# Kernel tuning notes

Measured on AMD Instinct MI355X. Metric: run time of the kernel, lower is better.

## Reference

```python
import jax, jax.numpy as jnp
import numpy as np

NUM_HEADS = 8
ATTN_LEN = 5


def setup_inputs() -> dict:
    rng = jax.random.key(0)
    ks = jax.random.split(rng, 10)
    B, T, D = 2, 4096, 1024
    H, HD = NUM_HEADS, D // NUM_HEADS
    n = lambda k, shape, scale=1.0: jax.random.normal(k, shape, jnp.float32) * scale
    return {
        "query": n(ks[0], (B, T, D)),
        "key": n(ks[1], (B, T, D)),
        "value": n(ks[2], (B, T, D)),
        "Wq": n(ks[3], (D, D), 0.02),
        "bq": jnp.zeros((D,), jnp.float32),
        "Wk": n(ks[4], (D, D), 0.02),
        "bk": jnp.zeros((D,), jnp.float32),
        "Wv": n(ks[5], (D, D), 0.02),
        "bv": jnp.zeros((D,), jnp.float32),
        "Er": n(ks[6], (H, HD, ATTN_LEN)),
        "layer": 1,
    }


def _forward(query, key, value, Wq, bq, Wk, bk, Wv, bv, Er, layer):
    B, T, D = query.shape
    H = NUM_HEADS
    HD = D // H
    dil = 2 ** layer
    pad = dil * (ATTN_LEN // 2)
    Tp = T + 2 * pad

    # torch nn.Linear: y = x @ W^T + b ; reshape to [B, H, T, HD]
    q = (query @ Wq.T + bq).reshape(B, T, H, HD).transpose(0, 2, 1, 3)
    k = (key @ Wk.T + bk).reshape(B, T, H, HD).transpose(0, 2, 1, 3)
    v = (value @ Wv.T + bv).reshape(B, T, H, HD).transpose(0, 2, 1, 3)

    # head-group source mapping + shifts (note k head 7 reuses k head 6, per source)
    src_k = jnp.array([0, 1, 2, 3, 4, 5, 6, 6])
    src_v = jnp.array([0, 1, 2, 3, 4, 5, 6, 7])
    shifts = jnp.array([0, 0, 0, 0, -2, -1, 1, 2])

    # kv_roll equivalence: window slot j at time t for shift s reads
    # padded[(t + (s + j) * dil) mod Tp]  (torch.roll wraparound included)
    t_idx = jnp.arange(T)
    j_idx = jnp.arange(ATTN_LEN)
    idx = (t_idx[None, :, None] + (shifts[:, None, None] + j_idx[None, None, :]) * dil) % Tp  # [H,T,L]

    def windows(x, src):
        xp = jnp.pad(x, ((0, 0), (0, 0), (pad, pad), (0, 0)))[:, src]  # [B,H,Tp,HD]
        g = jnp.take_along_axis(xp, idx.reshape(1, H, T * ATTN_LEN, 1), axis=2)
        return g.reshape(B, H, T, ATTN_LEN, HD)

    kw = windows(k, src_k)  # [B,H,T,L,HD]
    vw = windows(v, src_v)

    qk = jnp.einsum('bhtd,bhtjd->bhtj', q, kw)            # [B,H,T,L]
    mask = jnp.where(qk == 0.0, -jnp.inf, 0.0)            # zero dot product => padding
    qer = jnp.einsum('bhtd,hdj->bhtj', q, Er)             # relative positional bias
    attn = jax.nn.softmax((qk + qer) / np.sqrt(HD).astype(np.float32) + mask, axis=-1)
    out = jnp.einsum('bhtj,bhtjd->bhtd', attn, vw)        # [B,H,T,HD]
    out = out.transpose(0, 2, 1, 3).reshape(B, T, D)
    return out, attn[:, :, :, None, :]                     # attn shaped [B,H,T,1,L] like torch


def reference(query, key, value, Wq, bq, Wk, bk, Wv, bv, Er, layer):
    return _forward(query, key, value, Wq, bq, Wk, bk, Wv, bv, Er, layer)
```

## Files before the change

kernel.cpp:

```cpp
#include <hip/hip_runtime.h>
#include <hip/hip_bf16.h>

constexpr int B_ = 2, T_ = 4096, D_ = 1024, H_ = 8, HD_ = 128, L_ = 5;
constexpr int M_ = B_ * T_;
constexpr int K_ = D_;
constexpr int N_ = D_;
constexpr int TB_ = 64;
constexpr int NSMAX_ = 96;

typedef __attribute__((ext_vector_type(8))) __bf16 bf16x8;
typedef __attribute__((ext_vector_type(4))) float f32x4;

__device__ __constant__ int c_srck[8]  = {0, 1, 2, 3, 4, 5, 6, 6};
__device__ __constant__ int c_shift[8] = {0, 0, 0, 0, -2, -1, 1, 2};

__device__ __forceinline__ void gload_lds16(const void* g, void* l) {
    __builtin_amdgcn_global_load_lds(
        (__attribute__((address_space(1))) void*)g,
        (__attribute__((address_space(3))) void*)l, 16, 0, 0);
}

__global__ __launch_bounds__(256) void qkv_gemm_f32(
    const float* __restrict__ query,
    const float* __restrict__ key,
    const float* __restrict__ value,
    const float* __restrict__ Wq,
    const float* __restrict__ bq,
    const float* __restrict__ Wk,
    const float* __restrict__ bk,
    const float* __restrict__ Wv,
    const float* __restrict__ bv,
    __hip_bfloat16* __restrict__ qout,
    __hip_bfloat16* __restrict__ kout,
    __hip_bfloat16* __restrict__ vout)
{
    const int z = blockIdx.z;
    const float* A    = (z == 0) ? query : (z == 1) ? key : value;
    const float* W    = (z == 0) ? Wq    : (z == 1) ? Wk  : Wv;
    const float* bias = (z == 0) ? bq    : (z == 1) ? bk  : bv;
    __hip_bfloat16* C = (z == 0) ? qout  : (z == 1) ? kout : vout;

    __shared__ __align__(16) float As[128 * 32];
    __shared__ __align__(16) float Bs[128 * 32];

    const int tid  = threadIdx.x;
    const int wave = tid >> 6;
    const int lane = tid & 63;
    const int m0 = blockIdx.x * 128;
    const int n0 = blockIdx.y * 128;
    const int wm = (wave >> 1) * 64;
    const int wn = (wave & 1) * 64;

    f32x4 acc[4][4];
#pragma unroll
    for (int i = 0; i < 4; ++i)
#pragma unroll
        for (int j = 0; j < 4; ++j)
            acc[i][j] = (f32x4){0.f, 0.f, 0.f, 0.f};

    const int srow = lane >> 3;
    const int lcg  = (lane & 7) ^ srow;
    const int gcol = lcg * 4;

    const int fr  = lane & 15;
    const int r7  = fr & 7;
    const int cgA = (lane >> 4) * 2;
    const int pcg0 = (cgA)     ^ r7;
    const int pcg1 = (cgA ^ 1) ^ r7;

    for (int k0 = 0; k0 < K_; k0 += 32) {
#pragma unroll
        for (int r = 0; r < 4; ++r) {
            const int issue = wave + r * 4;
            const int row = issue * 8 + srow;
            gload_lds16(A + (size_t)(m0 + row) * K_ + k0 + gcol,
                        (void*)(As + issue * 256));
            gload_lds16(W + (size_t)(n0 + row) * K_ + k0 + gcol,
                        (void*)(Bs + issue * 256));
        }
        __syncthreads();

        bf16x8 af[4], bf[4];
#pragma unroll
        for (int i = 0; i < 4; ++i) {
            const float* ap = As + (wm + i * 16 + fr) * 32;
            f32x4 a0 = *(const f32x4*)(const void*)(ap + pcg0 * 4);
            f32x4 a1 = *(const f32x4*)(const void*)(ap + pcg1 * 4);
            const float* bp = Bs + (wn + i * 16 + fr) * 32;
            f32x4 b0 = *(const f32x4*)(const void*)(bp + pcg0 * 4);
            f32x4 b1 = *(const f32x4*)(const void*)(bp + pcg1 * 4);
#pragma unroll
            for (int e = 0; e < 4; ++e) {
                af[i][e]     = (__bf16)a0[e];
                af[i][e + 4] = (__bf16)a1[e];
                bf[i][e]     = (__bf16)b0[e];
                bf[i][e + 4] = (__bf16)b1[e];
            }
        }
#pragma unroll
        for (int i = 0; i < 4; ++i)
#pragma unroll
            for (int j = 0; j < 4; ++j)
                acc[i][j] = __builtin_amdgcn_mfma_f32_16x16x32_bf16(
                    af[i], bf[j], acc[i][j], 0, 0, 0);
        __syncthreads();
    }

    const int col_l = lane & 15;
    const int row_l = (lane >> 4) * 4;
#pragma unroll
    for (int j = 0; j < 4; ++j) {
        const int n = n0 + wn + j * 16 + col_l;
        const float bval = bias[n];
#pragma unroll
        for (int i = 0; i < 4; ++i) {
            const int m = m0 + wm + i * 16 + row_l;
#pragma unroll
            for (int r = 0; r < 4; ++r)
                C[(size_t)(m + r) * N_ + n] = __float2bfloat16(acc[i][j][r] + bval);
        }
    }
}

__global__ __launch_bounds__(256) void attn_kernel(
    const __hip_bfloat16* __restrict__ qp,
    const __hip_bfloat16* __restrict__ kp,
    const __hip_bfloat16* __restrict__ vp,
    const float* __restrict__ Er,
    const int* __restrict__ layer_p,
    float* __restrict__ out,
    float* __restrict__ attn_out)
{
    const int dil = 1 << (*layer_p);
    int NS = TB_ + 4 * dil;
    if (NS > NSMAX_) NS = NSMAX_;

    const int tid = threadIdx.x;
    const int t0 = blockIdx.x * TB_;
    const int h  = blockIdx.y;
    const int b  = blockIdx.z;
    const int shift = c_shift[h];
    const int srck  = c_srck[h];
    const int off_lo = (shift - 2) * dil;

    __shared__ __align__(16) __hip_bfloat16 Ks[NSMAX_ * 128];
    __shared__ __align__(16) __hip_bfloat16 Vs[NSMAX_ * 128];
    __shared__ __align__(16) float ErT[5][128];

    for (int i = tid; i < 640; i += 256) {
        const int d = i / 5, j = i - d * 5;
        ErT[j][d] = Er[(size_t)h * 640 + i];
    }

    const int sr = tid >> 4;
    const int sc = tid & 15;
    for (int i0 = 0; i0 < NS; i0 += 16) {
        const int i = i0 + sr;
        if (i < NS) {
            const int r = t0 + off_lo + i;
            bf16x8 kv8 = (bf16x8){0, 0, 0, 0, 0, 0, 0, 0};
            bf16x8 vv8 = (bf16x8){0, 0, 0, 0, 0, 0, 0, 0};
            if (r >= 0 && r < T_) {
                kv8 = *(const bf16x8*)(const void*)(
                    kp + (size_t)(b * T_ + r) * D_ + srck * HD_ + sc * 8);
                vv8 = *(const bf16x8*)(const void*)(
                    vp + (size_t)(b * T_ + r) * D_ + h * HD_ + sc * 8);
            }
            const int pc = sc ^ (i & 3);
            *(bf16x8*)(void*)(Ks + i * 128 + pc * 8) = kv8;
            *(bf16x8*)(void*)(Vs + i * 128 + pc * 8) = vv8;
        }
    }
    __syncthreads();

    const int lr = tid >> 2;
    const int ld = tid & 3;
    const int t  = t0 + lr;
    const size_t qoff = (size_t)(b * T_ + t) * D_ + h * HD_ + ld * 32;

    float qf[32];
#pragma unroll
    for (int c = 0; c < 4; ++c) {
        bf16x8 qv = *(const bf16x8*)(const void*)(qp + qoff + c * 8);
#pragma unroll
        for (int e = 0; e < 8; ++e) qf[c * 8 + e] = (float)qv[e];
    }

    float lg[5];
    bool  valid[5];
    int   irow[5];
#pragma unroll
    for (int j = 0; j < 5; ++j) {
        const int i = lr + j * dil;
        irow[j] = i;
        const int orig = t + (shift + j - 2) * dil;
        valid[j] = (orig >= 0) && (orig < T_);

        float s = 0.f;
#pragma unroll
        for (int c = 0; c < 4; ++c) {
            const int pc = (ld * 4 + c) ^ (i & 3);
            bf16x8 kk = *(const bf16x8*)(const void*)(Ks + i * 128 + pc * 8);
#pragma unroll
            for (int e = 0; e < 8; ++e) s += qf[c * 8 + e] * (float)kk[e];
        }
        if (!valid[j]) s = 0.f;
#pragma unroll
        for (int c = 0; c < 8; ++c) {
            f32x4 ev = *(const f32x4*)(const void*)(&ErT[j][ld * 32 + c * 4]);
#pragma unroll
            for (int e = 0; e < 4; ++e) s += qf[c * 4 + e] * ev[e];
        }
        s += __shfl_xor(s, 1, 4);
        s += __shfl_xor(s, 2, 4);
        lg[j] = valid[j] ? s * 0.08838834764831845f : -INFINITY;
    }

    float mx = lg[0];
#pragma unroll
    for (int j = 1; j < 5; ++j) mx = fmaxf(mx, lg[j]);
    float w[5], sum = 0.f;
#pragma unroll
    for (int j = 0; j < 5; ++j) {
        w[j] = valid[j] ? __expf(lg[j] - mx) : 0.f;
        sum += w[j];
    }
    const float inv = 1.f / sum;
#pragma unroll
    for (int j = 0; j < 5; ++j) w[j] *= inv;

    float o[32];
#pragma unroll
    for (int m = 0; m < 32; ++m) o[m] = 0.f;
#pragma unroll
    for (int j = 0; j < 5; ++j) {
        const int i = irow[j];
#pragma unroll
        for (int c = 0; c < 4; ++c) {
            const int pc = (ld * 4 + c) ^ (i & 3);
            bf16x8 vv = *(const bf16x8*)(const void*)(Vs + i * 128 + pc * 8);
#pragma unroll
            for (int e = 0; e < 8; ++e) o[c * 8 + e] += w[j] * (float)vv[e];
        }
    }

#pragma unroll
    for (int c = 0; c < 8; ++c) {
        f32x4 ov = (f32x4){o[c * 4], o[c * 4 + 1], o[c * 4 + 2], o[c * 4 + 3]};
        *(f32x4*)(void*)(out + qoff + c * 4) = ov;
    }

    const size_t abase = ((size_t)(b * H_ + h) * T_ + t) * L_;
    attn_out[abase + ld] = w[ld];
    if (ld == 0) attn_out[abase + 4] = w[4];
}

extern "C" void kernel_launch(void* const* d_in, const int* in_sizes, int n_in,
                              void* d_out, int out_size, void* d_ws, size_t ws_size,
                              hipStream_t stream) {
    const float* query = (const float*)d_in[0];
    const float* key   = (const float*)d_in[1];
    const float* value = (const float*)d_in[2];
    const float* Wq    = (const float*)d_in[3];
    const float* bq    = (const float*)d_in[4];
    const float* Wk    = (const float*)d_in[5];
    const float* bk    = (const float*)d_in[6];
    const float* Wv    = (const float*)d_in[7];
    const float* bv    = (const float*)d_in[8];
    const float* Er    = (const float*)d_in[9];
    const int*   layer = (const int*)d_in[10];

    float* out  = (float*)d_out;
    float* attn = out + (size_t)B_ * T_ * D_;

    const size_t SP = (size_t)M_ * N_;

    __hip_bfloat16* qp = (__hip_bfloat16*)d_ws;
    __hip_bfloat16* kp = qp + SP;
    __hip_bfloat16* vp = kp + SP;

    qkv_gemm_f32<<<dim3(M_ / 128, N_ / 128, 3), 256, 0, stream>>>(
        query, key, value, Wq, bq, Wk, bk, Wv, bv, qp, kp, vp);

    attn_kernel<<<dim3(T_ / TB_, H_, B_), 256, 0, stream>>>(
        qp, kp, vp, Er, layer, out, attn);
}
```

Before: 274.5 us.

## Convert GEMM operands to bf16 on staging and register-prefetch next K tile

The QKV GEMM no longer uses direct global-to-LDS fp32 loads. Each thread now loads the next K tile into registers while the current tile is computed, converts it to bf16 once, and writes it to LDS. This halves LDS footprint and LDS read traffic and removes the per-wave repeated fp32-to-bf16 conversion of MFMA fragments. In exchange it uses more registers and a plain bf16 LDS layout without the XOR swizzle, which may cause bank conflicts on fragment reads.

```diff
diff --git a/kernel.cpp b/kernel.cpp
--- a/kernel.cpp
+++ b/kernel.cpp
@@ -14,13 +14,7 @@
 __device__ __constant__ int c_srck[8]  = {0, 1, 2, 3, 4, 5, 6, 6};
 __device__ __constant__ int c_shift[8] = {0, 0, 0, 0, -2, -1, 1, 2};
 
-__device__ __forceinline__ void gload_lds16(const void* g, void* l) {
-    __builtin_amdgcn_global_load_lds(
-        (__attribute__((address_space(1))) void*)g,
-        (__attribute__((address_space(3))) void*)l, 16, 0, 0);
-}
-
-__global__ __launch_bounds__(256) void qkv_gemm_f32(
+__global__ __launch_bounds__(256) void qkv_gemm_fused(
     const float* __restrict__ query,
     const float* __restrict__ key,
     const float* __restrict__ value,
@@ -40,8 +34,8 @@
     const float* bias = (z == 0) ? bq    : (z == 1) ? bk  : bv;
     __hip_bfloat16* C = (z == 0) ? qout  : (z == 1) ? kout : vout;
 
-    __shared__ __align__(16) float As[128 * 32];
-    __shared__ __align__(16) float Bs[128 * 32];
+    __shared__ __align__(16) __hip_bfloat16 As[128 * 32];
+    __shared__ __align__(16) __hip_bfloat16 Bs[128 * 32];
 
     const int tid  = threadIdx.x;
     const int wave = tid >> 6;
@@ -58,44 +52,56 @@
         for (int j = 0; j < 4; ++j)
             acc[i][j] = (f32x4){0.f, 0.f, 0.f, 0.f};
 
-    const int srow = lane >> 3;
-    const int lcg  = (lane & 7) ^ srow;
-    const int gcol = lcg * 4;
-
-    const int fr  = lane & 15;
-    const int r7  = fr & 7;
-    const int cgA = (lane >> 4) * 2;
-    const int pcg0 = (cgA)     ^ r7;
-    const int pcg1 = (cgA ^ 1) ^ r7;
+    const int srow = lane >> 2;
+    const int scol = (lane & 3) * 8;
+
+    const int fr = lane & 15;
+    const int fk = (lane >> 4) * 8;
+
+    f32x4 rA[2][2], rW[2][2];
+
+    auto loadRegs = [&](int k0) {
+#pragma unroll
+        for (int r = 0; r < 2; ++r) {
+            const int row = (wave + r * 4) * 16 + srow;
+            const float* pa = A + (size_t)(m0 + row) * K_ + k0 + scol;
+            const float* pw = W + (size_t)(n0 + row) * K_ + k0 + scol;
+            rA[r][0] = *(const f32x4*)(const void*)pa;
+            rA[r][1] = *(const f32x4*)(const void*)(pa + 4);
+            rW[r][0] = *(const f32x4*)(const void*)pw;
+            rW[r][1] = *(const f32x4*)(const void*)(pw + 4);
+        }
+    };
+    auto writeLds = [&]() {
+#pragma unroll
+        for (int r = 0; r < 2; ++r) {
+            const int issue = wave + r * 4;
+            bf16x8 oa, ow;
+#pragma unroll
+            for (int e = 0; e < 4; ++e) {
+                oa[e]     = (__bf16)rA[r][0][e];
+                oa[e + 4] = (__bf16)rA[r][1][e];
+                ow[e]     = (__bf16)rW[r][0][e];
+                ow[e + 4] = (__bf16)rW[r][1][e];
+            }
+            *(bf16x8*)(void*)(As + issue * 512 + lane * 8) = oa;
+            *(bf16x8*)(void*)(Bs + issue * 512 + lane * 8) = ow;
+        }
+    };
+
+    loadRegs(0);
 
     for (int k0 = 0; k0 < K_; k0 += 32) {
-#pragma unroll
-        for (int r = 0; r < 4; ++r) {
-            const int issue = wave + r * 4;
-            const int row = issue * 8 + srow;
-            gload_lds16(A + (size_t)(m0 + row) * K_ + k0 + gcol,
-                        (void*)(As + issue * 256));
-            gload_lds16(W + (size_t)(n0 + row) * K_ + k0 + gcol,
-                        (void*)(Bs + issue * 256));
-        }
+        writeLds();
         __syncthreads();
 
+        if (k0 + 32 < K_) loadRegs(k0 + 32);
+
         bf16x8 af[4], bf[4];
 #pragma unroll
         for (int i = 0; i < 4; ++i) {
-            const float* ap = As + (wm + i * 16 + fr) * 32;
-            f32x4 a0 = *(const f32x4*)(const void*)(ap + pcg0 * 4);
-            f32x4 a1 = *(const f32x4*)(const void*)(ap + pcg1 * 4);
-            const float* bp = Bs + (wn + i * 16 + fr) * 32;
-            f32x4 b0 = *(const f32x4*)(const void*)(bp + pcg0 * 4);
-            f32x4 b1 = *(const f32x4*)(const void*)(bp + pcg1 * 4);
-#pragma unroll
-            for (int e = 0; e < 4; ++e) {
-                af[i][e]     = (__bf16)a0[e];
-                af[i][e + 4] = (__bf16)a1[e];
-                bf[i][e]     = (__bf16)b0[e];
-                bf[i][e + 4] = (__bf16)b1[e];
-            }
+            af[i] = *(const bf16x8*)(const void*)(As + (wm + i * 16 + fr) * 32 + fk);
+            bf[i] = *(const bf16x8*)(const void*)(Bs + (wn + i * 16 + fr) * 32 + fk);
         }
 #pragma unroll
         for (int i = 0; i < 4; ++i)
@@ -279,7 +285,7 @@
     __hip_bfloat16* kp = qp + SP;
     __hip_bfloat16* vp = kp + SP;
 
-    qkv_gemm_f32<<<dim3(M_ / 128, N_ / 128, 3), 256, 0, stream>>>(
+    qkv_gemm_fused<<<dim3(M_ / 128, N_ / 128, 3), 256, 0, stream>>>(
         query, key, value, Wq, bq, Wk, bk, Wv, bv, qp, kp, vp);
 
     attn_kernel<<<dim3(T_ / TB_, H_, B_), 256, 0, stream>>>(
```

Measured after the change: 274.8 us. Within noise of the previous version (+0.1%).
